# Performance work log

Hardware: AMD Instinct MI355X
Metric: run time of the kernel (lower is better)

Reference implementation:

```python
import jax, jax.numpy as jnp
import numpy as np

EPS = 1e-4   # synsin-style z clamp in world_to_view
BIG = 1e10   # z-buffer init


def _xy_grid(h, w):
    xs = jnp.linspace(-1.0, 1.0, w)
    ys = jnp.linspace(-1.0, 1.0, h)
    gy, gx = jnp.meshgrid(ys, xs, indexing='ij')
    return jnp.stack([gx.ravel(), gy.ravel()], 0)  # [2, h*w], NDC pixel rays


def _view_to_world(depth, K_inv, RTinv, xy):
    # depth [B,1,N]; homogeneous coords rows = (x*d, y*d, d, 1)
    proj = jnp.concatenate([xy[None] * depth, depth, jnp.ones_like(depth)], axis=1)  # [B,4,N]
    cam = jnp.einsum('bij,bjn->bin', K_inv, proj)
    return jnp.einsum('bij,bjn->bin', RTinv, cam)  # [B,4,N]


def _world_to_view(world, K, RT):
    cam2 = jnp.einsum('bij,bjn->bin', RT, world)
    xy_proj = jnp.einsum('bij,bjn->bin', K, cam2)
    z = xy_proj[:, 2:3]
    mask = jnp.abs(z) < EPS
    zs = jnp.where(mask, EPS, z)
    sampler = jnp.concatenate([xy_proj[:, 0:2] / zs, z], axis=1)  # [B,3,N]
    return jnp.where(mask, -10.0, sampler)


def _splat_one(sampler, feats, h, w):
    # sampler [3,N] (x,y in NDC, z depth); feats [C,N]. Nearest-pixel z-buffer splat.
    x, y, z = sampler[0], sampler[1], sampler[2]
    n = x.shape[0]
    px = jnp.round((x + 1.0) * 0.5 * (w - 1)).astype(jnp.int32)
    py = jnp.round((y + 1.0) * 0.5 * (h - 1)).astype(jnp.int32)
    valid = (px >= 0) & (px < w) & (py >= 0) & (py < h) & (z > EPS)
    idx = jnp.where(valid, py * w + px, h * w)  # invalid -> dump bucket h*w
    zv = jnp.where(valid, z, BIG)
    zbuf = jnp.full(h * w + 1, BIG, feats.dtype).at[idx].min(zv)
    pid = jnp.where(valid & (zv <= zbuf[idx]), jnp.arange(n, dtype=jnp.int32), n)
    win = jnp.full(h * w + 1, n, jnp.int32).at[idx].min(pid)[: h * w]  # winning point per pixel
    fpad = jnp.concatenate([feats, jnp.zeros((feats.shape[0], 1), feats.dtype)], axis=1)
    out = fpad[:, win].reshape(feats.shape[0], h, w)
    zb = zbuf[: h * w]
    depth = jnp.where(zb < BIG, zb, 0.0).reshape(1, h, w)
    return out, depth


def _project(depths, colors, feats, K, src_RTs, src_RTinvs, dst_RTs, dst_RTinvs):
    B, V, _, Hc, Wc = depths.shape
    _, _, C, Hf, Wf = feats.shape
    sh, sw = Hf / Hc, Wf / Wc
    scale = jnp.array([sw, sh, 1.0, 1.0], depths.dtype)[None, :, None]
    sK = K * scale
    sKinv = jnp.linalg.inv(sK)

    colors_r = jax.image.resize(colors.reshape(B * V, 3, Hc, Wc), (B * V, 3, Hf, Wf),
                                method='linear', antialias=True)
    depths_r = jax.image.resize(depths.reshape(B * V, 1, Hc, Wc), (B * V, 1, Hf, Wf),
                                method='nearest')
    feats_f = feats.reshape(B, V, C, Hf * Wf)
    colors_f = colors_r.reshape(B, V, 3, Hf * Wf)
    depths_f = depths_r.reshape(B, V, 1, Hf * Wf)

    xy = _xy_grid(Hf, Wf)
    dstRT = dst_RTs[:, 0]  # num_outputs == 1
    splat = jax.vmap(lambda s, f: _splat_one(s, f, Hf, Wf))

    results, warped, pdepths = [], [], []
    for i in range(V):  # small fixed number of source views
        world = _view_to_world(depths_f[:, i], sKinv, src_RTinvs[:, i], xy)
        sampler = _world_to_view(world, sK, dstRT)            # [B,3,N]
        src = jnp.concatenate([feats_f[:, i], colors_f[:, i] * 0.5 + 0.5], axis=1)  # [B,C+3,N]
        res, dep = splat(sampler, src)                        # [B,C+3,Hf,Wf], [B,1,Hf,Wf]
        results.append(res[:, :C])
        warped.append(res[:, C:])
        pdepths.append(dep)

    prj_fs = jnp.stack(results, 0)      # [V,B,C,Hf,Wf]
    warped = jnp.stack(warped, 0)       # [V,B,3,Hf,Wf]
    prj_depths = jnp.stack(pdepths, 0)  # [V,B,1,Hf,Wf]
    # forward() permutes prj_fs / prj_depths to [B,V,...]; warped stays [V,B,...]
    return prj_fs.transpose(1, 0, 2, 3, 4), warped, prj_depths.transpose(1, 0, 2, 3, 4)


def setup_inputs() -> dict:
    key = jax.random.key(0)
    k1, k2, k3 = jax.random.split(key, 3)
    B, V, Hc, Wc = 2, 2, 512, 512
    Hf, Wf, C = 256, 256, 64

    depths = jax.random.uniform(k1, (B, V, 1, Hc, Wc), jnp.float32, 1.0, 5.0)
    colors = jax.random.uniform(k2, (B, V, 3, Hc, Wc), jnp.float32, -1.0, 1.0)
    feats = jax.random.normal(k3, (B, V, C, Hf, Wf), jnp.float32)

    K = np.eye(4, dtype=np.float32)  # NDC intrinsic (fx=fy=1, cx=cy=0)
    th = 0.1
    R = np.array([[np.cos(th), 0, np.sin(th), 0.2],
                  [0, 1, 0, 0.0],
                  [-np.sin(th), 0, np.cos(th), 0.1],
                  [0, 0, 0, 1]], dtype=np.float32)
    src_RT = np.eye(4, dtype=np.float32)

    Kb = jnp.asarray(np.tile(K[None], (B, 1, 1)))
    src_RTs = jnp.asarray(np.tile(src_RT[None, None], (B, V, 1, 1)))
    src_RTinvs = src_RTs  # identity
    dst_RTs = jnp.asarray(np.tile(R[None, None], (B, 1, 1, 1)))
    dst_RTinvs = jnp.asarray(np.tile(np.linalg.inv(R)[None, None], (B, 1, 1, 1)))

    return {"depths": depths, "colors": colors, "feats": feats, "K": Kb,
            "src_RTs": src_RTs, "src_RTinvs": src_RTinvs,
            "dst_RTs": dst_RTs, "dst_RTinvs": dst_RTinvs}


def reference(depths, colors, feats, K, src_RTs, src_RTinvs, dst_RTs, dst_RTinvs):
    return _project(depths, colors, feats, K, src_RTs, src_RTinvs, dst_RTs, dst_RTinvs)
```

## Files before the change

### kernel.cpp

```cpp
#include <hip/hip_runtime.h>
#include <stdint.h>

#pragma clang fp contract(off)

namespace {
constexpr int B_ = 2, V_ = 2, HC = 512, WC = 512, HF = 256, WF = 256, CF = 64;
constexpr int NPIX = HF * WF;
constexpr float EPSF = 1e-4f;
constexpr float BIGF = 1e10f;
constexpr int NPT = B_ * V_ * NPIX;
constexpr int NBLK_PT = NPT / 256;
constexpr int RESIZE_BLKS = (B_ * V_ * 3 * NPIX) / 256;
constexpr int TP_BLKS = B_ * V_ * (NPIX / 64);
constexpr size_t WS_BASE = (size_t)NPT * 8 + (size_t)B_ * V_ * 3 * NPIX * 4 + 256;
constexpr size_t TF_BYTES = (size_t)NPT * CF * 4;
}

__device__ __forceinline__ float dot4f(const float* __restrict__ r,
                                       float v0, float v1, float v2, float v3) {
  float t = r[0] * v0;
  t = t + r[1] * v1;
  t = t + r[2] * v2;
  t = t + r[3] * v3;
  return t;
}

__global__ void init_k(const float* __restrict__ K,
                       float* __restrict__ mats,
                       unsigned long long* __restrict__ zwin) {
  int g = blockIdx.x * blockDim.x + threadIdx.x;
  zwin[g] = ~0ULL;

  if (g < B_) {
    int b = g;
    const float rowscale[4] = {0.5f, 0.5f, 1.0f, 1.0f};
    float sK[16];
    for (int i = 0; i < 4; ++i)
      for (int j = 0; j < 4; ++j)
        sK[i*4+j] = K[b*16 + i*4 + j] * rowscale[i];
    double m[16];
    for (int i = 0; i < 16; ++i) m[i] = (double)sK[i];
    double inv[16];
    inv[0]  =  m[5]*m[10]*m[15] - m[5]*m[11]*m[14] - m[9]*m[6]*m[15] + m[9]*m[7]*m[14] + m[13]*m[6]*m[11] - m[13]*m[7]*m[10];
    inv[4]  = -m[4]*m[10]*m[15] + m[4]*m[11]*m[14] + m[8]*m[6]*m[15] - m[8]*m[7]*m[14] - m[12]*m[6]*m[11] + m[12]*m[7]*m[10];
    inv[8]  =  m[4]*m[9]*m[15]  - m[4]*m[11]*m[13] - m[8]*m[5]*m[15] + m[8]*m[7]*m[13] + m[12]*m[5]*m[11] - m[12]*m[7]*m[9];
    inv[12] = -m[4]*m[9]*m[14]  + m[4]*m[10]*m[13] + m[8]*m[5]*m[14] - m[8]*m[6]*m[13] - m[12]*m[5]*m[10] + m[12]*m[6]*m[9];
    inv[1]  = -m[1]*m[10]*m[15] + m[1]*m[11]*m[14] + m[9]*m[2]*m[15] - m[9]*m[3]*m[14] - m[13]*m[2]*m[11] + m[13]*m[3]*m[10];
    inv[5]  =  m[0]*m[10]*m[15] - m[0]*m[11]*m[14] - m[8]*m[2]*m[15] + m[8]*m[3]*m[14] + m[12]*m[2]*m[11] - m[12]*m[3]*m[10];
    inv[9]  = -m[0]*m[9]*m[15]  + m[0]*m[11]*m[13] + m[8]*m[1]*m[15] - m[8]*m[3]*m[13] - m[12]*m[1]*m[11] + m[12]*m[3]*m[9];
    inv[13] =  m[0]*m[9]*m[14]  - m[0]*m[10]*m[13] - m[8]*m[1]*m[14] + m[8]*m[2]*m[13] + m[12]*m[1]*m[10] - m[12]*m[2]*m[9];
    inv[2]  =  m[1]*m[6]*m[15]  - m[1]*m[7]*m[14]  - m[5]*m[2]*m[15] + m[5]*m[3]*m[14] + m[13]*m[2]*m[7]  - m[13]*m[3]*m[6];
    inv[6]  = -m[0]*m[6]*m[15]  + m[0]*m[7]*m[14]  + m[4]*m[2]*m[15] - m[4]*m[3]*m[14] - m[12]*m[2]*m[7]  + m[12]*m[3]*m[6];
    inv[10] =  m[0]*m[5]*m[15]  - m[0]*m[7]*m[13]  - m[4]*m[1]*m[15] + m[4]*m[3]*m[13] + m[12]*m[1]*m[7]  - m[12]*m[3]*m[5];
    inv[14] = -m[0]*m[5]*m[14]  + m[0]*m[6]*m[13]  + m[4]*m[1]*m[14] - m[4]*m[2]*m[13] - m[12]*m[1]*m[6]  + m[12]*m[2]*m[5];
    inv[3]  = -m[1]*m[6]*m[11]  + m[1]*m[7]*m[10]  + m[5]*m[2]*m[11] - m[5]*m[3]*m[10] - m[9]*m[2]*m[7]   + m[9]*m[3]*m[6];
    inv[7]  =  m[0]*m[6]*m[11]  - m[0]*m[7]*m[10]  - m[4]*m[2]*m[11] + m[4]*m[3]*m[10] + m[8]*m[2]*m[7]   - m[8]*m[3]*m[6];
    inv[11] = -m[0]*m[5]*m[11]  + m[0]*m[7]*m[9]   + m[4]*m[1]*m[11] - m[4]*m[3]*m[9]  - m[8]*m[1]*m[7]   + m[8]*m[3]*m[5];
    inv[15] =  m[0]*m[5]*m[10]  - m[0]*m[6]*m[9]   - m[4]*m[1]*m[10] + m[4]*m[2]*m[9]  + m[8]*m[1]*m[6]   - m[8]*m[2]*m[5];
    double det = m[0]*inv[0] + m[1]*inv[4] + m[2]*inv[8] + m[3]*inv[12];
    double idet = 1.0 / det;
    for (int i = 0; i < 16; ++i) {
      mats[b*32 + i]      = sK[i];
      mats[b*32 + 16 + i] = (float)(inv[i] * idet);
    }
  }
}

__global__ void work_k(const float* __restrict__ depths,
                       const float* __restrict__ mats,
                       const float* __restrict__ srcRTinv,
                       const float* __restrict__ dstRT,
                       unsigned long long* __restrict__ zwin,
                       const float* __restrict__ feats,
                       float* __restrict__ tf,
                       const float* __restrict__ colors,
                       float* __restrict__ colr) {
  int bid = blockIdx.x;
  int nTP = (int)gridDim.x - RESIZE_BLKS - NBLK_PT;
  int t = threadIdx.x;

  if (bid < nTP) {
    int bv = bid >> 10;
    int pix0 = (bid & 1023) << 6;
    int c4 = t >> 4;
    int p4 = t & 15;
    const float* fb = feats + (size_t)bv * CF * NPIX + pix0 + 4 * p4;
    float4 v0 = *(const float4*)(fb + (size_t)(4 * c4 + 0) * NPIX);
    float4 v1 = *(const float4*)(fb + (size_t)(4 * c4 + 1) * NPIX);
    float4 v2 = *(const float4*)(fb + (size_t)(4 * c4 + 2) * NPIX);
    float4 v3 = *(const float4*)(fb + (size_t)(4 * c4 + 3) * NPIX);
    float* tb = tf + ((size_t)bv * NPIX + pix0 + 4 * p4) * CF + 4 * c4;
    *(float4*)(tb + 0 * CF) = make_float4(v0.x, v1.x, v2.x, v3.x);
    *(float4*)(tb + 1 * CF) = make_float4(v0.y, v1.y, v2.y, v3.y);
    *(float4*)(tb + 2 * CF) = make_float4(v0.z, v1.z, v2.z, v3.z);
    *(float4*)(tb + 3 * CF) = make_float4(v0.w, v1.w, v2.w, v3.w);
    return;
  }

  int rb = bid - nTP;
  if (rb < RESIZE_BLKS) {
    int g = rb * 256 + t;
    int pc  = g >> 16;
    int pix = g & (NPIX - 1);
    int y = pix >> 8, x = pix & (WF - 1);
    const float* src = colors + (size_t)pc * HC * WC;
    const float W37 = (float)(3.0 / 7.0), W17 = (float)(1.0 / 7.0);
    float wy[4] = {0.125f, 0.375f, 0.375f, 0.125f};
    float wx[4] = {0.125f, 0.375f, 0.375f, 0.125f};
    if (y == 0)      { wy[0] = 0.f; wy[1] = W37; wy[2] = W37; wy[3] = W17; }
    if (y == HF - 1) { wy[0] = W17; wy[1] = W37; wy[2] = W37; wy[3] = 0.f; }
    if (x == 0)      { wx[0] = 0.f; wx[1] = W37; wx[2] = W37; wx[3] = W17; }
    if (x == WF - 1) { wx[0] = W17; wx[1] = W37; wx[2] = W37; wx[3] = 0.f; }
    int jy0 = 2 * y - 1, jx0 = 2 * x - 1;
    float acc = 0.f;
    #pragma unroll
    for (int ty = 0; ty < 4; ++ty) {
      if (wy[ty] == 0.f) continue;
      int jy = jy0 + ty;
      float rs = 0.f;
      #pragma unroll
      for (int tx = 0; tx < 4; ++tx) {
        if (wx[tx] == 0.f) continue;
        rs = rs + wx[tx] * src[(size_t)jy * WC + (jx0 + tx)];
      }
      acc = acc + wy[ty] * rs;
    }
    colr[g] = acc;
    return;
  }

  int g = (rb - RESIZE_BLKS) * 256 + t;
  if (g >= NPT) return;
  int bv = g >> 16;
  int n  = g & (NPIX - 1);
  int b  = bv / V_;
  int y = n >> 8, x = n & (WF - 1);
  float d = depths[(size_t)bv * HC * WC + (size_t)(2 * y + 1) * WC + (2 * x + 1)];
  const float step32 = 2.0f / 255.0f;
  float xf = (float)x * step32 - 1.0f;
  float yf = (float)y * step32 - 1.0f;
  float pr0 = xf * d, pr1 = yf * d, pr2 = d, pr3 = 1.0f;
  const float* sK  = mats + b * 32;
  const float* sKi = mats + b * 32 + 16;
  const float* Rs  = srcRTinv + (size_t)bv * 16;
  const float* Rd  = dstRT + (size_t)b * 16;
  float a0 = dot4f(sKi + 0,  pr0, pr1, pr2, pr3);
  float a1 = dot4f(sKi + 4,  pr0, pr1, pr2, pr3);
  float a2 = dot4f(sKi + 8,  pr0, pr1, pr2, pr3);
  float a3 = dot4f(sKi + 12, pr0, pr1, pr2, pr3);
  float w0 = dot4f(Rs + 0,  a0, a1, a2, a3);
  float w1 = dot4f(Rs + 4,  a0, a1, a2, a3);
  float w2 = dot4f(Rs + 8,  a0, a1, a2, a3);
  float w3 = dot4f(Rs + 12, a0, a1, a2, a3);
  float c0 = dot4f(Rd + 0,  w0, w1, w2, w3);
  float c1 = dot4f(Rd + 4,  w0, w1, w2, w3);
  float c2 = dot4f(Rd + 8,  w0, w1, w2, w3);
  float c3 = dot4f(Rd + 12, w0, w1, w2, w3);
  float p0 = dot4f(sK + 0, c0, c1, c2, c3);
  float p1 = dot4f(sK + 4, c0, c1, c2, c3);
  float p2 = dot4f(sK + 8, c0, c1, c2, c3);
  if (!(p2 > EPSF)) return;
  float sx = p0 / p2, sy = p1 / p2;
  float pxf = rintf(((sx + 1.0f) * 0.5f) * 255.0f);
  float pyf = rintf(((sy + 1.0f) * 0.5f) * 255.0f);
  if (!(pxf >= 0.0f && pxf <= 255.0f && pyf >= 0.0f && pyf <= 255.0f)) return;
  int idx = (int)pyf * WF + (int)pxf;
  unsigned zbits = __float_as_uint(p2);
  unsigned long long key = ((unsigned long long)zbits << 32) | (unsigned)n;
  atomicMin(&zwin[(size_t)bv * NPIX + idx], key);
}

__global__ void gather3_k(const unsigned long long* __restrict__ zwin,
                          const float* __restrict__ tf,
                          const float* __restrict__ colr,
                          float* __restrict__ out0,
                          float* __restrict__ out1,
                          float* __restrict__ out2) {
  int bid = blockIdx.x;
  int grp = bid >> 10;
  int g   = (bid & (NBLK_PT - 1)) * 256 + threadIdx.x;
  int bv  = g >> 16;
  int pix = g & (NPIX - 1);
  unsigned long long key = zwin[g];
  bool hit = (key != ~0ULL);
  int n = (int)(key & 0xffffffffULL);

  if (grp < 2) {
    float4 f[8];
    if (hit) {
      const float4* src =
          (const float4*)(tf + ((size_t)bv * NPIX + n) * CF + grp * 32);
      #pragma unroll
      for (int i = 0; i < 8; ++i) f[i] = src[i];
    } else {
      #pragma unroll
      for (int i = 0; i < 8; ++i) f[i] = make_float4(0.f, 0.f, 0.f, 0.f);
    }
    float* o0 = out0 + (size_t)bv * CF * NPIX + (size_t)(grp * 32) * NPIX + pix;
    const float* fs = (const float*)f;
    #pragma unroll
    for (int c = 0; c < 32; ++c)
      __builtin_nontemporal_store(fs[c], &o0[(size_t)c * NPIX]);
  } else {
    int b = bv >> 1, v = bv & 1;
    const float* cb = colr + (size_t)bv * 3 * NPIX;
    float* o1 = out1 + (size_t)(v * B_ + b) * 3 * NPIX + pix;
    if (hit) {
      float z = __uint_as_float((unsigned)(key >> 32));
      __builtin_nontemporal_store((z < BIGF) ? z : 0.0f, &out2[g]);
      #pragma unroll
      for (int ch = 0; ch < 3; ++ch)
        __builtin_nontemporal_store(cb[(size_t)ch * NPIX + n] * 0.5f + 0.5f,
                                    &o1[(size_t)ch * NPIX]);
    } else {
      __builtin_nontemporal_store(0.0f, &out2[g]);
      #pragma unroll
      for (int ch = 0; ch < 3; ++ch)
        __builtin_nontemporal_store(0.0f, &o1[(size_t)ch * NPIX]);
    }
  }
}

__global__ void gather_k(const unsigned long long* __restrict__ zwin,
                         const float* __restrict__ feats,
                         const float* __restrict__ colr,
                         float* __restrict__ out0,
                         float* __restrict__ out1,
                         float* __restrict__ out2) {
  int bid = blockIdx.x;
  int grp = bid >> 10;
  int g   = (bid & (NBLK_PT - 1)) * 256 + threadIdx.x;
  int bv  = g >> 16;
  int pix = g & (NPIX - 1);
  unsigned long long key = zwin[g];
  bool hit = (key != ~0ULL);
  int n = (int)(key & 0xffffffffULL);

  if (grp < 4) {
    int c0 = grp * 16;
    const float* fb = feats + (size_t)bv * CF * NPIX + (size_t)c0 * NPIX;
    float* o0 = out0 + (size_t)bv * CF * NPIX + (size_t)c0 * NPIX + pix;
    if (hit) {
      #pragma unroll
      for (int c = 0; c < 16; ++c)
        __builtin_nontemporal_store(fb[(size_t)c * NPIX + n], &o0[(size_t)c * NPIX]);
    } else {
      #pragma unroll
      for (int c = 0; c < 16; ++c)
        __builtin_nontemporal_store(0.0f, &o0[(size_t)c * NPIX]);
    }
  } else {
    int b = bv >> 1, v = bv & 1;
    const float* cb = colr + (size_t)bv * 3 * NPIX;
    float* o1 = out1 + (size_t)(v * B_ + b) * 3 * NPIX + pix;
    if (hit) {
      float z = __uint_as_float((unsigned)(key >> 32));
      __builtin_nontemporal_store((z < BIGF) ? z : 0.0f, &out2[g]);
      #pragma unroll
      for (int ch = 0; ch < 3; ++ch)
        __builtin_nontemporal_store(cb[(size_t)ch * NPIX + n] * 0.5f + 0.5f,
                                    &o1[(size_t)ch * NPIX]);
    } else {
      __builtin_nontemporal_store(0.0f, &out2[g]);
      #pragma unroll
      for (int ch = 0; ch < 3; ++ch)
        __builtin_nontemporal_store(0.0f, &o1[(size_t)ch * NPIX]);
    }
  }
}

extern "C" void kernel_launch(void* const* d_in, const int* in_sizes, int n_in,
                              void* d_out, int out_size, void* d_ws, size_t ws_size,
                              hipStream_t stream) {
  const float* depths     = (const float*)d_in[0];
  const float* colors     = (const float*)d_in[1];
  const float* feats      = (const float*)d_in[2];
  const float* K          = (const float*)d_in[3];
  const float* src_RTinvs = (const float*)d_in[5];
  const float* dst_RTs    = (const float*)d_in[6];

  float* out0 = (float*)d_out;
  float* out1 = out0 + (size_t)B_ * V_ * CF * NPIX;
  float* out2 = out1 + (size_t)V_ * B_ * 3 * NPIX;

  unsigned long long* zwin = (unsigned long long*)d_ws;
  float* colr = (float*)(zwin + NPT);
  float* mats = colr + (size_t)B_ * V_ * 3 * NPIX;
  float* tf   = (float*)((char*)d_ws + WS_BASE);

  const bool use_tf = (ws_size >= WS_BASE + TF_BYTES);

  init_k<<<NBLK_PT, 256, 0, stream>>>(K, mats, zwin);
  int work_grid = (use_tf ? TP_BLKS : 0) + RESIZE_BLKS + NBLK_PT;
  work_k<<<work_grid, 256, 0, stream>>>(depths, mats, src_RTinvs, dst_RTs, zwin,
                                        feats, tf, colors, colr);
  if (use_tf)
    gather3_k<<<3 * NBLK_PT, 256, 0, stream>>>(zwin, tf, colr, out0, out1, out2);
  else
    gather_k<<<5 * NBLK_PT, 256, 0, stream>>>(zwin, feats, colr, out0, out1, out2);
}
```

Baseline: 181.5 us.

## Fuse init, transpose, resize, splat and gather into one cooperative kernel

Result: slower. 434.6 us (+139.4%).

```diff
diff --git a/kernel.cpp b/kernel.cpp
--- a/kernel.cpp
+++ b/kernel.cpp
@@ -1,7 +1,10 @@
 #include <hip/hip_runtime.h>
+#include <hip/hip_cooperative_groups.h>
 #include <stdint.h>
 
 #pragma clang fp contract(off)
+
+namespace cg = cooperative_groups;
 
 namespace {
 constexpr int B_ = 2, V_ = 2, HC = 512, WC = 512, HF = 256, WF = 256, CF = 64;
@@ -9,7 +12,7 @@
 constexpr float EPSF = 1e-4f;
 constexpr float BIGF = 1e10f;
 constexpr int NPT = B_ * V_ * NPIX;
-constexpr int NBLK_PT = NPT / 256;
+constexpr int NBLK = 1024;
 constexpr int RESIZE_BLKS = (B_ * V_ * 3 * NPIX) / 256;
 constexpr int TP_BLKS = B_ * V_ * (NPIX / 64);
 constexpr size_t WS_BASE = (size_t)NPT * 8 + (size_t)B_ * V_ * 3 * NPIX * 4 + 256;
@@ -25,112 +28,96 @@
   return t;
 }
 
-__global__ void init_k(const float* __restrict__ K,
-                       float* __restrict__ mats,
-                       unsigned long long* __restrict__ zwin) {
-  int g = blockIdx.x * blockDim.x + threadIdx.x;
-  zwin[g] = ~0ULL;
-
-  if (g < B_) {
-    int b = g;
-    const float rowscale[4] = {0.5f, 0.5f, 1.0f, 1.0f};
-    float sK[16];
-    for (int i = 0; i < 4; ++i)
-      for (int j = 0; j < 4; ++j)
-        sK[i*4+j] = K[b*16 + i*4 + j] * rowscale[i];
-    double m[16];
-    for (int i = 0; i < 16; ++i) m[i] = (double)sK[i];
-    double inv[16];
-    inv[0]  =  m[5]*m[10]*m[15] - m[5]*m[11]*m[14] - m[9]*m[6]*m[15] + m[9]*m[7]*m[14] + m[13]*m[6]*m[11] - m[13]*m[7]*m[10];
-    inv[4]  = -m[4]*m[10]*m[15] + m[4]*m[11]*m[14] + m[8]*m[6]*m[15] - m[8]*m[7]*m[14] - m[12]*m[6]*m[11] + m[12]*m[7]*m[10];
-    inv[8]  =  m[4]*m[9]*m[15]  - m[4]*m[11]*m[13] - m[8]*m[5]*m[15] + m[8]*m[7]*m[13] + m[12]*m[5]*m[11] - m[12]*m[7]*m[9];
-    inv[12] = -m[4]*m[9]*m[14]  + m[4]*m[10]*m[13] + m[8]*m[5]*m[14] - m[8]*m[6]*m[13] - m[12]*m[5]*m[10] + m[12]*m[6]*m[9];
-    inv[1]  = -m[1]*m[10]*m[15] + m[1]*m[11]*m[14] + m[9]*m[2]*m[15] - m[9]*m[3]*m[14] - m[13]*m[2]*m[11] + m[13]*m[3]*m[10];
-    inv[5]  =  m[0]*m[10]*m[15] - m[0]*m[11]*m[14] - m[8]*m[2]*m[15] + m[8]*m[3]*m[14] + m[12]*m[2]*m[11] - m[12]*m[3]*m[10];
-    inv[9]  = -m[0]*m[9]*m[15]  + m[0]*m[11]*m[13] + m[8]*m[1]*m[15] - m[8]*m[3]*m[13] - m[12]*m[1]*m[11] + m[12]*m[3]*m[9];
-    inv[13] =  m[0]*m[9]*m[14]  - m[0]*m[10]*m[13] - m[8]*m[1]*m[14] + m[8]*m[2]*m[13] + m[12]*m[1]*m[10] - m[12]*m[2]*m[9];
-    inv[2]  =  m[1]*m[6]*m[15]  - m[1]*m[7]*m[14]  - m[5]*m[2]*m[15] + m[5]*m[3]*m[14] + m[13]*m[2]*m[7]  - m[13]*m[3]*m[6];
-    inv[6]  = -m[0]*m[6]*m[15]  + m[0]*m[7]*m[14]  + m[4]*m[2]*m[15] - m[4]*m[3]*m[14] - m[12]*m[2]*m[7]  + m[12]*m[3]*m[6];
-    inv[10] =  m[0]*m[5]*m[15]  - m[0]*m[7]*m[13]  - m[4]*m[1]*m[15] + m[4]*m[3]*m[13] + m[12]*m[1]*m[7]  - m[12]*m[3]*m[5];
-    inv[14] = -m[0]*m[5]*m[14]  + m[0]*m[6]*m[13]  + m[4]*m[1]*m[14] - m[4]*m[2]*m[13] - m[12]*m[1]*m[6]  + m[12]*m[2]*m[5];
-    inv[3]  = -m[1]*m[6]*m[11]  + m[1]*m[7]*m[10]  + m[5]*m[2]*m[11] - m[5]*m[3]*m[10] - m[9]*m[2]*m[7]   + m[9]*m[3]*m[6];
-    inv[7]  =  m[0]*m[6]*m[11]  - m[0]*m[7]*m[10]  - m[4]*m[2]*m[11] + m[4]*m[3]*m[10] + m[8]*m[2]*m[7]   - m[8]*m[3]*m[6];
-    inv[11] = -m[0]*m[5]*m[11]  + m[0]*m[7]*m[9]   + m[4]*m[1]*m[11] - m[4]*m[3]*m[9]  - m[8]*m[1]*m[7]   + m[8]*m[3]*m[5];
-    inv[15] =  m[0]*m[5]*m[10]  - m[0]*m[6]*m[9]   - m[4]*m[1]*m[10] + m[4]*m[2]*m[9]  + m[8]*m[1]*m[6]   - m[8]*m[2]*m[5];
-    double det = m[0]*inv[0] + m[1]*inv[4] + m[2]*inv[8] + m[3]*inv[12];
-    double idet = 1.0 / det;
-    for (int i = 0; i < 16; ++i) {
-      mats[b*32 + i]      = sK[i];
-      mats[b*32 + 16 + i] = (float)(inv[i] * idet);
-    }
-  }
-}
-
-__global__ void work_k(const float* __restrict__ depths,
-                       const float* __restrict__ mats,
-                       const float* __restrict__ srcRTinv,
-                       const float* __restrict__ dstRT,
-                       unsigned long long* __restrict__ zwin,
-                       const float* __restrict__ feats,
-                       float* __restrict__ tf,
-                       const float* __restrict__ colors,
-                       float* __restrict__ colr) {
-  int bid = blockIdx.x;
-  int nTP = (int)gridDim.x - RESIZE_BLKS - NBLK_PT;
-  int t = threadIdx.x;
-
-  if (bid < nTP) {
-    int bv = bid >> 10;
-    int pix0 = (bid & 1023) << 6;
-    int c4 = t >> 4;
-    int p4 = t & 15;
-    const float* fb = feats + (size_t)bv * CF * NPIX + pix0 + 4 * p4;
-    float4 v0 = *(const float4*)(fb + (size_t)(4 * c4 + 0) * NPIX);
-    float4 v1 = *(const float4*)(fb + (size_t)(4 * c4 + 1) * NPIX);
-    float4 v2 = *(const float4*)(fb + (size_t)(4 * c4 + 2) * NPIX);
-    float4 v3 = *(const float4*)(fb + (size_t)(4 * c4 + 3) * NPIX);
-    float* tb = tf + ((size_t)bv * NPIX + pix0 + 4 * p4) * CF + 4 * c4;
-    *(float4*)(tb + 0 * CF) = make_float4(v0.x, v1.x, v2.x, v3.x);
-    *(float4*)(tb + 1 * CF) = make_float4(v0.y, v1.y, v2.y, v3.y);
-    *(float4*)(tb + 2 * CF) = make_float4(v0.z, v1.z, v2.z, v3.z);
-    *(float4*)(tb + 3 * CF) = make_float4(v0.w, v1.w, v2.w, v3.w);
-    return;
-  }
-
-  int rb = bid - nTP;
-  if (rb < RESIZE_BLKS) {
-    int g = rb * 256 + t;
-    int pc  = g >> 16;
-    int pix = g & (NPIX - 1);
-    int y = pix >> 8, x = pix & (WF - 1);
-    const float* src = colors + (size_t)pc * HC * WC;
-    const float W37 = (float)(3.0 / 7.0), W17 = (float)(1.0 / 7.0);
-    float wy[4] = {0.125f, 0.375f, 0.375f, 0.125f};
-    float wx[4] = {0.125f, 0.375f, 0.375f, 0.125f};
-    if (y == 0)      { wy[0] = 0.f; wy[1] = W37; wy[2] = W37; wy[3] = W17; }
-    if (y == HF - 1) { wy[0] = W17; wy[1] = W37; wy[2] = W37; wy[3] = 0.f; }
-    if (x == 0)      { wx[0] = 0.f; wx[1] = W37; wx[2] = W37; wx[3] = W17; }
-    if (x == WF - 1) { wx[0] = W17; wx[1] = W37; wx[2] = W37; wx[3] = 0.f; }
-    int jy0 = 2 * y - 1, jx0 = 2 * x - 1;
-    float acc = 0.f;
-    #pragma unroll
-    for (int ty = 0; ty < 4; ++ty) {
-      if (wy[ty] == 0.f) continue;
-      int jy = jy0 + ty;
-      float rs = 0.f;
-      #pragma unroll
-      for (int tx = 0; tx < 4; ++tx) {
-        if (wx[tx] == 0.f) continue;
-        rs = rs + wx[tx] * src[(size_t)jy * WC + (jx0 + tx)];
-      }
-      acc = acc + wy[ty] * rs;
-    }
-    colr[g] = acc;
-    return;
-  }
-
-  int g = (rb - RESIZE_BLKS) * 256 + t;
-  if (g >= NPT) return;
+__device__ void mats_compute(const float* __restrict__ K, int b,
+                             float* __restrict__ mats) {
+  const float rowscale[4] = {0.5f, 0.5f, 1.0f, 1.0f};
+  float sK[16];
+  for (int i = 0; i < 4; ++i)
+    for (int j = 0; j < 4; ++j)
+      sK[i*4+j] = K[b*16 + i*4 + j] * rowscale[i];
+  double m[16];
+  for (int i = 0; i < 16; ++i) m[i] = (double)sK[i];
+  double inv[16];
+  inv[0]  =  m[5]*m[10]*m[15] - m[5]*m[11]*m[14] - m[9]*m[6]*m[15] + m[9]*m[7]*m[14] + m[13]*m[6]*m[11] - m[13]*m[7]*m[10];
+  inv[4]  = -m[4]*m[10]*m[15] + m[4]*m[11]*m[14] + m[8]*m[6]*m[15] - m[8]*m[7]*m[14] - m[12]*m[6]*m[11] + m[12]*m[7]*m[10];
+  inv[8]  =  m[4]*m[9]*m[15]  - m[4]*m[11]*m[13] - m[8]*m[5]*m[15] + m[8]*m[7]*m[13] + m[12]*m[5]*m[11] - m[12]*m[7]*m[9];
+  inv[12] = -m[4]*m[9]*m[14]  + m[4]*m[10]*m[13] + m[8]*m[5]*m[14] - m[8]*m[6]*m[13] - m[12]*m[5]*m[10] + m[12]*m[6]*m[9];
+  inv[1]  = -m[1]*m[10]*m[15] + m[1]*m[11]*m[14] + m[9]*m[2]*m[15] - m[9]*m[3]*m[14] - m[13]*m[2]*m[11] + m[13]*m[3]*m[10];
+  inv[5]  =  m[0]*m[10]*m[15] - m[0]*m[11]*m[14] - m[8]*m[2]*m[15] + m[8]*m[3]*m[14] + m[12]*m[2]*m[11] - m[12]*m[3]*m[10];
+  inv[9]  = -m[0]*m[9]*m[15]  + m[0]*m[11]*m[13] + m[8]*m[1]*m[15] - m[8]*m[3]*m[13] - m[12]*m[1]*m[11] + m[12]*m[3]*m[9];
+  inv[13] =  m[0]*m[9]*m[14]  - m[0]*m[10]*m[13] - m[8]*m[1]*m[14] + m[8]*m[2]*m[13] + m[12]*m[1]*m[10] - m[12]*m[2]*m[9];
+  inv[2]  =  m[1]*m[6]*m[15]  - m[1]*m[7]*m[14]  - m[5]*m[2]*m[15] + m[5]*m[3]*m[14] + m[13]*m[2]*m[7]  - m[13]*m[3]*m[6];
+  inv[6]  = -m[0]*m[6]*m[15]  + m[0]*m[7]*m[14]  + m[4]*m[2]*m[15] - m[4]*m[3]*m[14] - m[12]*m[2]*m[7]  + m[12]*m[3]*m[6];
+  inv[10] =  m[0]*m[5]*m[15]  - m[0]*m[7]*m[13]  - m[4]*m[1]*m[15] + m[4]*m[3]*m[13] + m[12]*m[1]*m[7]  - m[12]*m[3]*m[5];
+  inv[14] = -m[0]*m[5]*m[14]  + m[0]*m[6]*m[13]  + m[4]*m[1]*m[14] - m[4]*m[2]*m[13] - m[12]*m[1]*m[6]  + m[12]*m[2]*m[5];
+  inv[3]  = -m[1]*m[6]*m[11]  + m[1]*m[7]*m[10]  + m[5]*m[2]*m[11] - m[5]*m[3]*m[10] - m[9]*m[2]*m[7]   + m[9]*m[3]*m[6];
+  inv[7]  =  m[0]*m[6]*m[11]  - m[0]*m[7]*m[10]  - m[4]*m[2]*m[11] + m[4]*m[3]*m[10] + m[8]*m[2]*m[7]   - m[8]*m[3]*m[6];
+  inv[11] = -m[0]*m[5]*m[11]  + m[0]*m[7]*m[9]   + m[4]*m[1]*m[11] - m[4]*m[3]*m[9]  - m[8]*m[1]*m[7]   + m[8]*m[3]*m[5];
+  inv[15] =  m[0]*m[5]*m[10]  - m[0]*m[6]*m[9]   - m[4]*m[1]*m[10] + m[4]*m[2]*m[9]  + m[8]*m[1]*m[6]   - m[8]*m[2]*m[5];
+  double det = m[0]*inv[0] + m[1]*inv[4] + m[2]*inv[8] + m[3]*inv[12];
+  double idet = 1.0 / det;
+  for (int i = 0; i < 16; ++i) {
+    mats[b*32 + i]      = sK[i];
+    mats[b*32 + 16 + i] = (float)(inv[i] * idet);
+  }
+}
+
+__device__ __forceinline__ void transp_tile(int tid, int t,
+                                            const float* __restrict__ feats,
+                                            float* __restrict__ tf) {
+  int bv = tid >> 10;
+  int pix0 = (tid & 1023) << 6;
+  int c4 = t >> 4;
+  int p4 = t & 15;
+  const float* fb = feats + (size_t)bv * CF * NPIX + pix0 + 4 * p4;
+  float4 v0 = *(const float4*)(fb + (size_t)(4 * c4 + 0) * NPIX);
+  float4 v1 = *(const float4*)(fb + (size_t)(4 * c4 + 1) * NPIX);
+  float4 v2 = *(const float4*)(fb + (size_t)(4 * c4 + 2) * NPIX);
+  float4 v3 = *(const float4*)(fb + (size_t)(4 * c4 + 3) * NPIX);
+  float* tb = tf + ((size_t)bv * NPIX + pix0 + 4 * p4) * CF + 4 * c4;
+  *(float4*)(tb + 0 * CF) = make_float4(v0.x, v1.x, v2.x, v3.x);
+  *(float4*)(tb + 1 * CF) = make_float4(v0.y, v1.y, v2.y, v3.y);
+  *(float4*)(tb + 2 * CF) = make_float4(v0.z, v1.z, v2.z, v3.z);
+  *(float4*)(tb + 3 * CF) = make_float4(v0.w, v1.w, v2.w, v3.w);
+}
+
+__device__ __forceinline__ void resize_body(int g,
+                                            const float* __restrict__ colors,
+                                            float* __restrict__ colr) {
+  int pc  = g >> 16;
+  int pix = g & (NPIX - 1);
+  int y = pix >> 8, x = pix & (WF - 1);
+  const float* src = colors + (size_t)pc * HC * WC;
+  const float W37 = (float)(3.0 / 7.0), W17 = (float)(1.0 / 7.0);
+  float wy[4] = {0.125f, 0.375f, 0.375f, 0.125f};
+  float wx[4] = {0.125f, 0.375f, 0.375f, 0.125f};
+  if (y == 0)      { wy[0] = 0.f; wy[1] = W37; wy[2] = W37; wy[3] = W17; }
+  if (y == HF - 1) { wy[0] = W17; wy[1] = W37; wy[2] = W37; wy[3] = 0.f; }
+  if (x == 0)      { wx[0] = 0.f; wx[1] = W37; wx[2] = W37; wx[3] = W17; }
+  if (x == WF - 1) { wx[0] = W17; wx[1] = W37; wx[2] = W37; wx[3] = 0.f; }
+  int jy0 = 2 * y - 1, jx0 = 2 * x - 1;
+  float acc = 0.f;
+  #pragma unroll
+  for (int ty = 0; ty < 4; ++ty) {
+    if (wy[ty] == 0.f) continue;
+    int jy = jy0 + ty;
+    float rs = 0.f;
+    #pragma unroll
+    for (int tx = 0; tx < 4; ++tx) {
+      if (wx[tx] == 0.f) continue;
+      rs = rs + wx[tx] * src[(size_t)jy * WC + (jx0 + tx)];
+    }
+    acc = acc + wy[ty] * rs;
+  }
+  colr[g] = acc;
+}
+
+__device__ __forceinline__ void splat_body(int g,
+                                           const float* __restrict__ depths,
+                                           const float* __restrict__ mats,
+                                           const float* __restrict__ srcRTinv,
+                                           const float* __restrict__ dstRT,
+                                           unsigned long long* __restrict__ zwin) {
   int bv = g >> 16;
   int n  = g & (NPIX - 1);
   int b  = bv / V_;
@@ -159,15 +146,114 @@
   float p0 = dot4f(sK + 0, c0, c1, c2, c3);
   float p1 = dot4f(sK + 4, c0, c1, c2, c3);
   float p2 = dot4f(sK + 8, c0, c1, c2, c3);
-  if (!(p2 > EPSF)) return;
-  float sx = p0 / p2, sy = p1 / p2;
-  float pxf = rintf(((sx + 1.0f) * 0.5f) * 255.0f);
-  float pyf = rintf(((sy + 1.0f) * 0.5f) * 255.0f);
-  if (!(pxf >= 0.0f && pxf <= 255.0f && pyf >= 0.0f && pyf <= 255.0f)) return;
-  int idx = (int)pyf * WF + (int)pxf;
-  unsigned zbits = __float_as_uint(p2);
-  unsigned long long key = ((unsigned long long)zbits << 32) | (unsigned)n;
-  atomicMin(&zwin[(size_t)bv * NPIX + idx], key);
+  if (p2 > EPSF) {
+    float sx = p0 / p2, sy = p1 / p2;
+    float pxf = rintf(((sx + 1.0f) * 0.5f) * 255.0f);
+    float pyf = rintf(((sy + 1.0f) * 0.5f) * 255.0f);
+    if (pxf >= 0.0f && pxf <= 255.0f && pyf >= 0.0f && pyf <= 255.0f) {
+      int idx = (int)pyf * WF + (int)pxf;
+      unsigned zbits = __float_as_uint(p2);
+      unsigned long long key = ((unsigned long long)zbits << 32) | (unsigned)n;
+      atomicMin(&zwin[(size_t)bv * NPIX + idx], key);
+    }
+  }
+}
+
+__device__ __forceinline__ void gather_point(int g, unsigned long long key,
+                                             const float* __restrict__ tf,
+                                             const float* __restrict__ colr,
+                                             float* __restrict__ out0,
+                                             float* __restrict__ out1,
+                                             float* __restrict__ out2) {
+  int bv = g >> 16;
+  int pix = g & (NPIX - 1);
+  bool hit = (key != ~0ULL);
+  int n = (int)(key & 0xffffffffULL);
+  float4 f[16];
+  if (hit) {
+    const float4* src = (const float4*)(tf + ((size_t)bv * NPIX + n) * CF);
+    #pragma unroll
+    for (int i = 0; i < 16; ++i) f[i] = src[i];
+  } else {
+    #pragma unroll
+    for (int i = 0; i < 16; ++i) f[i] = make_float4(0.f, 0.f, 0.f, 0.f);
+  }
+  float* o0 = out0 + (size_t)bv * CF * NPIX + pix;
+  const float* fs = (const float*)f;
+  #pragma unroll
+  for (int c = 0; c < CF; ++c)
+    __builtin_nontemporal_store(fs[c], &o0[(size_t)c * NPIX]);
+
+  int b = bv >> 1, v = bv & 1;
+  const float* cb = colr + (size_t)bv * 3 * NPIX;
+  float* o1 = out1 + (size_t)(v * B_ + b) * 3 * NPIX + pix;
+  if (hit) {
+    float z = __uint_as_float((unsigned)(key >> 32));
+    __builtin_nontemporal_store((z < BIGF) ? z : 0.0f, &out2[g]);
+    #pragma unroll
+    for (int ch = 0; ch < 3; ++ch)
+      __builtin_nontemporal_store(cb[(size_t)ch * NPIX + n] * 0.5f + 0.5f,
+                                  &o1[(size_t)ch * NPIX]);
+  } else {
+    __builtin_nontemporal_store(0.0f, &out2[g]);
+    #pragma unroll
+    for (int ch = 0; ch < 3; ++ch)
+      __builtin_nontemporal_store(0.0f, &o1[(size_t)ch * NPIX]);
+  }
+}
+
+__global__ __launch_bounds__(256, 4) void mega_k(
+    const float* __restrict__ depths, const float* __restrict__ colors,
+    const float* __restrict__ feats, const float* __restrict__ K,
+    const float* __restrict__ srcRTinv, const float* __restrict__ dstRT,
+    float* __restrict__ out0, float* __restrict__ out1,
+    float* __restrict__ out2, unsigned long long* __restrict__ zwin,
+    float* __restrict__ colr, float* __restrict__ mats,
+    float* __restrict__ tf) {
+  int bid = blockIdx.x, t = threadIdx.x;
+  int g0 = bid * 256 + t;
+
+  zwin[g0] = ~0ULL;
+  if (g0 < B_) mats_compute(K, g0, mats);
+  #pragma unroll
+  for (int i = 0; i < 4; ++i) transp_tile(i * NBLK + bid, t, feats, tf);
+  #pragma unroll
+  for (int i = 0; i < 3; ++i) resize_body((i * NBLK + bid) * 256 + t, colors, colr);
+
+  cg::this_grid().sync();
+
+  splat_body(g0, depths, mats, srcRTinv, dstRT, zwin);
+
+  cg::this_grid().sync();
+
+  gather_point(g0, zwin[g0], tf, colr, out0, out1, out2);
+}
+
+__global__ void init_k(const float* __restrict__ K,
+                       float* __restrict__ mats,
+                       unsigned long long* __restrict__ zwin) {
+  int g = blockIdx.x * blockDim.x + threadIdx.x;
+  zwin[g] = ~0ULL;
+  if (g < B_) mats_compute(K, g, mats);
+}
+
+__global__ void work_k(const float* __restrict__ depths,
+                       const float* __restrict__ mats,
+                       const float* __restrict__ srcRTinv,
+                       const float* __restrict__ dstRT,
+                       unsigned long long* __restrict__ zwin,
+                       const float* __restrict__ feats,
+                       float* __restrict__ tf,
+                       const float* __restrict__ colors,
+                       float* __restrict__ colr) {
+  int bid = blockIdx.x;
+  int nTP = (int)gridDim.x - RESIZE_BLKS - NBLK;
+  int t = threadIdx.x;
+  if (bid < nTP) { transp_tile(bid, t, feats, tf); return; }
+  int rb = bid - nTP;
+  if (rb < RESIZE_BLKS) { resize_body(rb * 256 + t, colors, colr); return; }
+  int g = (rb - RESIZE_BLKS) * 256 + t;
+  splat_body(g, depths, mats, srcRTinv, dstRT, zwin);
 }
 
 __global__ void gather3_k(const unsigned long long* __restrict__ zwin,
@@ -178,7 +264,7 @@
                           float* __restrict__ out2) {
   int bid = blockIdx.x;
   int grp = bid >> 10;
-  int g   = (bid & (NBLK_PT - 1)) * 256 + threadIdx.x;
+  int g   = (bid & (NBLK - 1)) * 256 + threadIdx.x;
   int bv  = g >> 16;
   int pix = g & (NPIX - 1);
   unsigned long long key = zwin[g];
@@ -229,7 +315,7 @@
                          float* __restrict__ out2) {
   int bid = blockIdx.x;
   int grp = bid >> 10;
-  int g   = (bid & (NBLK_PT - 1)) * 256 + threadIdx.x;
+  int g   = (bid & (NBLK - 1)) * 256 + threadIdx.x;
   int bv  = g >> 16;
   int pix = g & (NPIX - 1);
   unsigned long long key = zwin[g];
@@ -290,12 +376,23 @@
 
   const bool use_tf = (ws_size >= WS_BASE + TF_BYTES);
 
-  init_k<<<NBLK_PT, 256, 0, stream>>>(K, mats, zwin);
-  int work_grid = (use_tf ? TP_BLKS : 0) + RESIZE_BLKS + NBLK_PT;
+  if (use_tf) {
+    void* kargs[] = {(void*)&depths, (void*)&colors, (void*)&feats, (void*)&K,
+                     (void*)&src_RTinvs, (void*)&dst_RTs, (void*)&out0,
+                     (void*)&out1, (void*)&out2, (void*)&zwin, (void*)&colr,
+                     (void*)&mats, (void*)&tf};
+    hipError_t err = hipLaunchCooperativeKernel((const void*)mega_k, dim3(NBLK),
+                                                dim3(256), kargs, 0, stream);
+    if (err == hipSuccess) return;
+    (void)hipGetLastError();
+  }
+
+  init_k<<<NBLK, 256, 0, stream>>>(K, mats, zwin);
+  int work_grid = (use_tf ? TP_BLKS : 0) + RESIZE_BLKS + NBLK;
   work_k<<<work_grid, 256, 0, stream>>>(depths, mats, src_RTinvs, dst_RTs, zwin,
                                         feats, tf, colors, colr);
   if (use_tf)
-    gather3_k<<<3 * NBLK_PT, 256, 0, stream>>>(zwin, tf, colr, out0, out1, out2);
+    gather3_k<<<3 * NBLK, 256, 0, stream>>>(zwin, tf, colr, out0, out1, out2);
   else
-    gather_k<<<5 * NBLK_PT, 256, 0, stream>>>(zwin, feats, colr, out0, out1, out2);
-}
+    gather_k<<<5 * NBLK, 256, 0, stream>>>(zwin, feats, colr, out0, out1, out2);
+}
```
